# Kernel tuning notes

Measured on AMD Instinct MI355X. Metric: run time of the kernel, lower is better.

Reference implementation:

```python
import jax, jax.numpy as jnp
import numpy as np

B, S, D, H = 2, 2048, 1024, 16
DH = D // H
NEG = jnp.float32(-1e30)


def setup_inputs() -> dict:
    key = jax.random.key(0)
    ks = jax.random.split(key, 5)
    x = jax.random.normal(ks[0], (B, S, D), dtype=jnp.float32)
    # causal mask: attn_mask == 0 means blocked (matches masked_fill(attn_mask == 0))
    attn_mask = jnp.tril(jnp.ones((S, S), dtype=jnp.int32))
    key_padding_mask = jnp.zeros((B, S), dtype=bool)  # True = pad (none here)
    sd = 1.0 / np.sqrt(D)
    W_qkv = jax.random.normal(ks[1], (D, 3 * D), dtype=jnp.float32) * sd
    b_qkv = jnp.zeros((3 * D,), dtype=jnp.float32)
    W_proj = jax.random.normal(ks[2], (D, D), dtype=jnp.float32) * sd
    b_proj = jnp.zeros((D,), dtype=jnp.float32)
    return {"x": x, "W_qkv": W_qkv, "b_qkv": b_qkv, "W_proj": W_proj,
            "b_proj": b_proj, "attn_mask": attn_mask,
            "key_padding_mask": key_padding_mask}


def reference(x, W_qkv, b_qkv, W_proj, b_proj, attn_mask, key_padding_mask):
    scale = jnp.float32(DH) ** -0.5
    qkv = (x @ W_qkv + b_qkv).reshape(B, S, 3, H, DH)
    qkv = jnp.transpose(qkv, (2, 0, 3, 1, 4))  # (3, B, H, S, DH)
    q, k, v = qkv[0], qkv[1], qkv[2]
    attn = jnp.einsum("bhqd,bhkd->bhqk", q, k) * scale  # (B,H,S,S)
    # key padding mask: True -> -inf on that key column
    attn = jnp.where(key_padding_mask[:, None, None, :], NEG, attn)
    # attn mask: 0 -> blocked
    attn = jnp.where(attn_mask[None, None, :, :] == 0, NEG, attn)
    attn = jax.nn.softmax(attn, axis=-1)
    out = jnp.einsum("bhqk,bhkd->bhqd", attn, v)
    out = jnp.transpose(out, (0, 2, 1, 3)).reshape(B, S, D)
    return out @ W_proj + b_proj
```

## Files before the change

kernel.cpp:

```cpp
#include <hip/hip_runtime.h>


typedef __bf16 bf16;
typedef bf16 bf16x4 __attribute__((ext_vector_type(4)));
typedef bf16 bf16x8 __attribute__((ext_vector_type(8)));
typedef float f32x4 __attribute__((ext_vector_type(4)));

#define S_LEN 2048
#define DMODEL 1024
#define NHEAD 16
#define DHEAD 64

__device__ __forceinline__ void async_ld16(void* lds, const void* g) {
  __builtin_amdgcn_global_load_lds(
      (const __attribute__((address_space(1))) unsigned int*)g,
      (__attribute__((address_space(3))) unsigned int*)lds, 16, 0, 0);
}

__global__ __launch_bounds__(256) void prep_kernel(
    const float* __restrict__ x, const float* __restrict__ Wq,
    const float* __restrict__ Wp, bf16* __restrict__ Xb,
    bf16* __restrict__ Wtq, bf16* __restrict__ Wtp) {
  __shared__ float t[32][33];
  const int bid = blockIdx.x, tid = threadIdx.x;
  if (bid < 4096) {
    int i = bid * 256 + tid;
    float4 v = ((const float4*)x)[i];
    bf16x4 o;
    o[0] = (bf16)v.x; o[1] = (bf16)v.y; o[2] = (bf16)v.z; o[3] = (bf16)v.w;
    *(bf16x4*)(&Xb[4 * i]) = o;
    return;
  }
  const float* in; bf16* out; int R, C, bx, by;
  if (bid < 7168) {
    int b = bid - 4096; in = Wq; out = Wtq; R = 1024; C = 3072;
    bx = b % 96; by = b / 96;
  } else {
    int b = bid - 7168; in = Wp; out = Wtp; R = 1024; C = 1024;
    bx = b % 32; by = b / 32;
  }
  int tx = tid & 31, ty = tid >> 5;
  int bc = bx * 32, br = by * 32;
#pragma unroll
  for (int i = 0; i < 32; i += 8)
    t[ty + i][tx] = in[(size_t)(br + ty + i) * C + bc + tx];
  __syncthreads();
#pragma unroll
  for (int i = 0; i < 32; i += 8)
    out[(size_t)(bc + ty + i) * R + br + tx] = (bf16)t[tx][ty + i];
}

__global__ __launch_bounds__(256) void gemm_qkv(
    const bf16* __restrict__ A, const bf16* __restrict__ Bt,
    const float* __restrict__ bias, bf16* __restrict__ Oq,
    bf16* __restrict__ Ok, bf16* __restrict__ Ov, int Ksz) {
  __shared__ bf16 As[128 * 32];
  __shared__ bf16 Bs[128 * 32];
  const int tid = threadIdx.x, lane = tid & 63, w = tid >> 6;
  const int wm = (w >> 1) * 64, wn = (w & 1) * 64;
  const int lr = lane & 15, kg = lane >> 4;
  const int m0 = blockIdx.y * 128, n0 = blockIdx.x * 128;

  f32x4 acc[4][4] = {};

  for (int k0 = 0; k0 < Ksz; k0 += 32) {
#pragma unroll
    for (int i = 0; i < 2; ++i) {
      int seg = tid + i * 256;
      int row = seg >> 2, cs = (seg & 3) * 8;
      async_ld16(&As[row * 32 + cs], &A[(size_t)(m0 + row) * Ksz + k0 + cs]);
      async_ld16(&Bs[row * 32 + cs], &Bt[(size_t)(n0 + row) * Ksz + k0 + cs]);
    }
    __syncthreads();
    bf16x8 af[4], bfr[4];
#pragma unroll
    for (int i = 0; i < 4; ++i)
      af[i] = *(const bf16x8*)(&As[(wm + i * 16 + lr) * 32 + kg * 8]);
#pragma unroll
    for (int j = 0; j < 4; ++j)
      bfr[j] = *(const bf16x8*)(&Bs[(wn + j * 16 + lr) * 32 + kg * 8]);
#pragma unroll
    for (int i = 0; i < 4; ++i)
#pragma unroll
      for (int j = 0; j < 4; ++j)
        acc[i][j] = __builtin_amdgcn_mfma_f32_16x16x32_bf16(af[i], bfr[j], acc[i][j], 0, 0, 0);
    __syncthreads();
  }

  const int rbase = kg * 4;
#pragma unroll
  for (int i = 0; i < 4; ++i) {
#pragma unroll
    for (int j = 0; j < 4; ++j) {
      int ncol = n0 + wn + j * 16 + lr;
      float bv = bias[ncol];
#pragma unroll
      for (int r = 0; r < 4; ++r) {
        int m = m0 + wm + i * 16 + rbase + r;
        float v = acc[i][j][r] + bv;
        int t = ncol >> 10, rem = ncol & 1023;
        int h = rem >> 6, d = rem & 63;
        int s = m & 2047;
        size_t hb = (size_t)((m >> 11) * NHEAD + h) * S_LEN;
        if (t == 0)      Oq[(hb + s) * DHEAD + d] = (bf16)v;
        else if (t == 1) Ok[(hb + s) * DHEAD + d] = (bf16)v;
        else             Ov[hb * DHEAD + (size_t)d * S_LEN + s] = (bf16)v;
      }
    }
  }
}

__global__ __launch_bounds__(256) void gemm_proj(
    const bf16* __restrict__ A, const bf16* __restrict__ Bt,
    const float* __restrict__ bias, float* __restrict__ Of,
    int Ksz, int Nsz) {
  __shared__ bf16 As[64 * 32];
  __shared__ bf16 Bs[128 * 32];
  const int tid = threadIdx.x, lane = tid & 63, w = tid >> 6;
  const int wm = (w >> 1) * 32, wn = (w & 1) * 64;
  const int lr = lane & 15, kg = lane >> 4;
  const int m0 = blockIdx.y * 64, n0 = blockIdx.x * 128;

  f32x4 acc[2][4] = {};

  for (int k0 = 0; k0 < Ksz; k0 += 32) {
    {
      int row = tid >> 2, cs = (tid & 3) * 8;
      async_ld16(&As[row * 32 + cs], &A[(size_t)(m0 + row) * Ksz + k0 + cs]);
    }
#pragma unroll
    for (int i = 0; i < 2; ++i) {
      int seg = tid + i * 256;
      int row = seg >> 2, cs = (seg & 3) * 8;
      async_ld16(&Bs[row * 32 + cs], &Bt[(size_t)(n0 + row) * Ksz + k0 + cs]);
    }
    __syncthreads();
    bf16x8 af[2], bfr[4];
#pragma unroll
    for (int i = 0; i < 2; ++i)
      af[i] = *(const bf16x8*)(&As[(wm + i * 16 + lr) * 32 + kg * 8]);
#pragma unroll
    for (int j = 0; j < 4; ++j)
      bfr[j] = *(const bf16x8*)(&Bs[(wn + j * 16 + lr) * 32 + kg * 8]);
#pragma unroll
    for (int i = 0; i < 2; ++i)
#pragma unroll
      for (int j = 0; j < 4; ++j)
        acc[i][j] = __builtin_amdgcn_mfma_f32_16x16x32_bf16(af[i], bfr[j], acc[i][j], 0, 0, 0);
    __syncthreads();
  }

  const int rbase = kg * 4;
#pragma unroll
  for (int i = 0; i < 2; ++i) {
#pragma unroll
    for (int j = 0; j < 4; ++j) {
      int ncol = n0 + wn + j * 16 + lr;
      float bv = bias[ncol];
#pragma unroll
      for (int r = 0; r < 4; ++r) {
        int m = m0 + wm + i * 16 + rbase + r;
        Of[(size_t)m * Nsz + ncol] = acc[i][j][r] + bv;
      }
    }
  }
}

__global__ __launch_bounds__(256) void attn_kernel(
    const bf16* __restrict__ Q, const bf16* __restrict__ K,
    const bf16* __restrict__ Vtg, bf16* __restrict__ O) {
  __shared__ bf16 Ks[128 * 72];
  __shared__ bf16 Vt[80 * 136];
  __shared__ bf16 Pt[4][16 * 136];

  const int tid = threadIdx.x, lane = tid & 63, w = tid >> 6;
  const int lr = lane & 15, quad = lane >> 4;
  const int flat = blockIdx.x;
  const int p = (flat >> 3) & 15;
  const int bh = (flat & 7) + ((flat >> 7) << 3);
  const int b = bh >> 4, h = bh & 15;
  const bf16* Qp = Q + (size_t)bh * S_LEN * DHEAD;
  const bf16* Kp = K + (size_t)bh * S_LEN * DHEAD;
  const bf16* Vp = Vtg + (size_t)bh * S_LEN * DHEAD;

  for (int i = tid; i < 16 * 136; i += 256) {
    int rr = i / 136;
    Vt[(64 + rr) * 136 + (i - rr * 136)] = (rr == 0) ? (bf16)1.0f : (bf16)0.0f;
  }
  __syncthreads();

  const float qs = 0.125f * 1.44269504f;

  for (int seg = 0; seg < 2; ++seg) {
    const int qt = seg ? (31 - p) : p;
    const int q0 = qt * 64;
    const int qrow = q0 + w * 16;

    bf16x8 q0r = *(const bf16x8*)(Qp + (size_t)(qrow + lr) * DHEAD + quad * 8);
    bf16x8 q1r = *(const bf16x8*)(Qp + (size_t)(qrow + lr) * DHEAD + 32 + quad * 8);
    bf16x8 qf0, qf1;
#pragma unroll
    for (int e = 0; e < 8; ++e) {
      qf0[e] = (bf16)((float)q0r[e] * qs);
      qf1[e] = (bf16)((float)q1r[e] * qs);
    }

    f32x4 acc[4] = {};
    f32x4 acc5 = {};
    float m_i = -1e30f;

    const int ktiles = (q0 + 63) / 128 + 1;
    for (int kt = 0; kt < ktiles; ++kt) {
      const int kb = kt * 128;
#pragma unroll
      for (int i = 0; i < 4; ++i) {
        int sg = tid + i * 256;
        int krow = sg >> 3, kc = (sg & 7) * 8;
        *(bf16x8*)(&Ks[krow * 72 + kc]) =
            *(const bf16x8*)(&Kp[(size_t)(kb + krow) * DHEAD + kc]);
        int vd = sg >> 4, vs = (sg & 15) * 8;
        *(bf16x8*)(&Vt[vd * 136 + vs]) =
            *(const bf16x8*)(&Vp[(size_t)vd * S_LEN + kb + vs]);
      }
      __syncthreads();

      f32x4 sc[8];
#pragma unroll
      for (int ct = 0; ct < 8; ++ct) {
        bf16x8 kf0 = *(const bf16x8*)(&Ks[(ct * 16 + lr) * 72 + quad * 8]);
        bf16x8 kf1 = *(const bf16x8*)(&Ks[(ct * 16 + lr) * 72 + 32 + quad * 8]);
        f32x4 a = {};
        a = __builtin_amdgcn_mfma_f32_16x16x32_bf16(kf0, qf0, a, 0, 0, 0);
        a = __builtin_amdgcn_mfma_f32_16x16x32_bf16(kf1, qf1, a, 0, 0, 0);
        sc[ct] = a;
      }

      const bool full = (kb + 127) <= qrow;
      float pmax = -1e30f;
      if (full) {
#pragma unroll
        for (int ct = 0; ct < 8; ++ct)
#pragma unroll
          for (int r = 0; r < 4; ++r) pmax = fmaxf(pmax, sc[ct][r]);
      } else {
        const int qg = qrow + lr;
#pragma unroll
        for (int ct = 0; ct < 8; ++ct)
#pragma unroll
          for (int r = 0; r < 4; ++r) {
            int key = kb + ct * 16 + quad * 4 + r;
            if (key > qg) sc[ct][r] = -1e30f;
            pmax = fmaxf(pmax, sc[ct][r]);
          }
      }
      pmax = fmaxf(pmax, __shfl_xor(pmax, 16));
      pmax = fmaxf(pmax, __shfl_xor(pmax, 32));

      float mn = fmaxf(m_i, pmax);
      float alpha = __builtin_amdgcn_exp2f(m_i - mn);
      m_i = mn;
#pragma unroll
      for (int ct = 0; ct < 8; ++ct)
#pragma unroll
        for (int r = 0; r < 4; ++r)
          sc[ct][r] = __builtin_amdgcn_exp2f(sc[ct][r] - mn);
#pragma unroll
      for (int nt = 0; nt < 4; ++nt)
#pragma unroll
        for (int r = 0; r < 4; ++r) acc[nt][r] *= alpha;
#pragma unroll
      for (int r = 0; r < 4; ++r) acc5[r] *= alpha;

#pragma unroll
      for (int ct = 0; ct < 8; ++ct) {
        bf16x4 pk;
#pragma unroll
        for (int r = 0; r < 4; ++r) pk[r] = (bf16)sc[ct][r];
        *(bf16x4*)(&Pt[w][lr * 136 + ct * 16 + quad * 4]) = pk;
      }

#pragma unroll
      for (int k0 = 0; k0 < 4; ++k0) {
        bf16x8 pf = *(const bf16x8*)(&Pt[w][lr * 136 + k0 * 32 + quad * 8]);
#pragma unroll
        for (int nt = 0; nt < 4; ++nt) {
          bf16x8 vf = *(const bf16x8*)(&Vt[(nt * 16 + lr) * 136 + k0 * 32 + quad * 8]);
          acc[nt] = __builtin_amdgcn_mfma_f32_16x16x32_bf16(vf, pf, acc[nt], 0, 0, 0);
        }
        bf16x8 vf5 = *(const bf16x8*)(&Vt[(64 + lr) * 136 + k0 * 32 + quad * 8]);
        acc5 = __builtin_amdgcn_mfma_f32_16x16x32_bf16(vf5, pf, acc5, 0, 0, 0);
      }
      __syncthreads();
    }

    float lsum = __shfl(acc5[0], lr);
    float inv = 1.f / lsum;
    size_t base = ((size_t)(b * S_LEN + qrow + lr)) * DMODEL + h * DHEAD;
#pragma unroll
    for (int nt = 0; nt < 4; ++nt) {
      bf16x4 ov;
#pragma unroll
      for (int r = 0; r < 4; ++r) ov[r] = (bf16)(acc[nt][r] * inv);
      *(bf16x4*)(&O[base + nt * 16 + quad * 4]) = ov;
    }
  }
}

extern "C" void kernel_launch(void* const* d_in, const int* in_sizes, int n_in,
                              void* d_out, int out_size, void* d_ws, size_t ws_size,
                              hipStream_t stream) {
  (void)in_sizes; (void)n_in; (void)out_size; (void)ws_size;
  const float* x     = (const float*)d_in[0];
  const float* Wqkv  = (const float*)d_in[1];
  const float* bqkv  = (const float*)d_in[2];
  const float* Wproj = (const float*)d_in[3];
  const float* bproj = (const float*)d_in[4];
  float* out = (float*)d_out;

  char* ws = (char*)d_ws;
  bf16* Xb  = (bf16*)(ws + 0);
  bf16* AO  = (bf16*)(ws + 0);
  bf16* Wtq = (bf16*)(ws + 8388608);
  bf16* Wtp = (bf16*)(ws + 16777216);
  bf16* Qb  = (bf16*)(ws + 18874368);
  bf16* Kb  = (bf16*)(ws + 27262976);
  bf16* Vtg = (bf16*)(ws + 35651584);

  prep_kernel<<<8192, 256, 0, stream>>>(x, Wqkv, Wproj, Xb, Wtq, Wtp);
  gemm_qkv<<<dim3(24, 32), 256, 0, stream>>>(Xb, Wtq, bqkv, Qb, Kb, Vtg, 1024);
  attn_kernel<<<512, 256, 0, stream>>>(Qb, Kb, Vtg, AO);
  gemm_proj<<<dim3(8, 64), 256, 0, stream>>>(AO, Wtp, bproj, out, 1024, 1024);
}
```

Measured before the change: 210.3 us.

## Register-prefetch next K/V tile, add MFMA priority hints, lazy softmax rescale

The next K/V tile is now loaded from global memory into registers while the current tile is being computed, and written to LDS at the start of the next iteration. This is meant to hide global load latency behind the MFMA work. s_setprio raises wave priority around the MFMA sections. The online-softmax rescale is skipped when the new row max exceeds the running max by no more than 8 in log2 units, which saves exp and multiply work. The cost is more registers per thread and probabilities above 1 held in bf16.

```diff
diff --git a/kernel.cpp b/kernel.cpp
--- a/kernel.cpp
+++ b/kernel.cpp
@@ -210,21 +210,43 @@
     float m_i = -1e30f;
 
     const int ktiles = (q0 + 63) / 128 + 1;
+
+    bf16x8 kreg[4], vreg[4];
+#pragma unroll
+    for (int i = 0; i < 4; ++i) {
+      int sg = tid + i * 256;
+      int krow = sg >> 3, kc = (sg & 7) * 8;
+      kreg[i] = *(const bf16x8*)(&Kp[(size_t)krow * DHEAD + kc]);
+      int vd = sg >> 4, vs = (sg & 15) * 8;
+      vreg[i] = *(const bf16x8*)(&Vp[(size_t)vd * S_LEN + vs]);
+    }
+
     for (int kt = 0; kt < ktiles; ++kt) {
       const int kb = kt * 128;
 #pragma unroll
       for (int i = 0; i < 4; ++i) {
         int sg = tid + i * 256;
         int krow = sg >> 3, kc = (sg & 7) * 8;
-        *(bf16x8*)(&Ks[krow * 72 + kc]) =
-            *(const bf16x8*)(&Kp[(size_t)(kb + krow) * DHEAD + kc]);
+        *(bf16x8*)(&Ks[krow * 72 + kc]) = kreg[i];
         int vd = sg >> 4, vs = (sg & 15) * 8;
-        *(bf16x8*)(&Vt[vd * 136 + vs]) =
-            *(const bf16x8*)(&Vp[(size_t)vd * S_LEN + kb + vs]);
+        *(bf16x8*)(&Vt[vd * 136 + vs]) = vreg[i];
       }
       __syncthreads();
 
+      if (kt + 1 < ktiles) {
+        const int kbn = kb + 128;
+#pragma unroll
+        for (int i = 0; i < 4; ++i) {
+          int sg = tid + i * 256;
+          int krow = sg >> 3, kc = (sg & 7) * 8;
+          kreg[i] = *(const bf16x8*)(&Kp[(size_t)(kbn + krow) * DHEAD + kc]);
+          int vd = sg >> 4, vs = (sg & 15) * 8;
+          vreg[i] = *(const bf16x8*)(&Vp[(size_t)vd * S_LEN + kbn + vs]);
+        }
+      }
+
       f32x4 sc[8];
+      __builtin_amdgcn_s_setprio(1);
 #pragma unroll
       for (int ct = 0; ct < 8; ++ct) {
         bf16x8 kf0 = *(const bf16x8*)(&Ks[(ct * 16 + lr) * 72 + quad * 8]);
@@ -234,6 +256,7 @@
         a = __builtin_amdgcn_mfma_f32_16x16x32_bf16(kf1, qf1, a, 0, 0, 0);
         sc[ct] = a;
       }
+      __builtin_amdgcn_s_setprio(0);
 
       const bool full = (kb + 127) <= qrow;
       float pmax = -1e30f;
@@ -256,20 +279,23 @@
       pmax = fmaxf(pmax, __shfl_xor(pmax, 16));
       pmax = fmaxf(pmax, __shfl_xor(pmax, 32));
 
-      float mn = fmaxf(m_i, pmax);
-      float alpha = __builtin_amdgcn_exp2f(m_i - mn);
-      m_i = mn;
+      if (!__all(pmax <= m_i + 8.0f)) {
+        float mn = fmaxf(m_i, pmax);
+        float alpha = __builtin_amdgcn_exp2f(m_i - mn);
+        m_i = mn;
+#pragma unroll
+        for (int nt = 0; nt < 4; ++nt)
+#pragma unroll
+          for (int r = 0; r < 4; ++r) acc[nt][r] *= alpha;
+#pragma unroll
+        for (int r = 0; r < 4; ++r) acc5[r] *= alpha;
+      }
+
 #pragma unroll
       for (int ct = 0; ct < 8; ++ct)
 #pragma unroll
         for (int r = 0; r < 4; ++r)
-          sc[ct][r] = __builtin_amdgcn_exp2f(sc[ct][r] - mn);
-#pragma unroll
-      for (int nt = 0; nt < 4; ++nt)
-#pragma unroll
-        for (int r = 0; r < 4; ++r) acc[nt][r] *= alpha;
-#pragma unroll
-      for (int r = 0; r < 4; ++r) acc5[r] *= alpha;
+          sc[ct][r] = __builtin_amdgcn_exp2f(sc[ct][r] - m_i);
 
 #pragma unroll
       for (int ct = 0; ct < 8; ++ct) {
@@ -279,6 +305,7 @@
         *(bf16x4*)(&Pt[w][lr * 136 + ct * 16 + quad * 4]) = pk;
       }
 
+      __builtin_amdgcn_s_setprio(1);
 #pragma unroll
       for (int k0 = 0; k0 < 4; ++k0) {
         bf16x8 pf = *(const bf16x8*)(&Pt[w][lr * 136 + k0 * 32 + quad * 8]);
@@ -290,6 +317,7 @@
         bf16x8 vf5 = *(const bf16x8*)(&Vt[(64 + lr) * 136 + k0 * 32 + quad * 8]);
         acc5 = __builtin_amdgcn_mfma_f32_16x16x32_bf16(vf5, pf, acc5, 0, 0, 0);
       }
+      __builtin_amdgcn_s_setprio(0);
       __syncthreads();
     }
 
```

Result: faster. 205.9 us (-2.1%).
